# Optimization experiments

Measured on AMD Instinct MI355X. Metric: run time of the kernel, lower is better.

## Reference

```python
import jax, jax.numpy as jnp
import numpy as np
from jax.ops import segment_sum

N = 50000        # nodes
E = 800000       # edges (avg degree 16)
H = 128          # hidden_dim
N_ITER = 2       # BCRefinement n_iterations
TIE_P = 0.05     # fraction of tie (boundary) edges


def setup_inputs() -> dict:
    key = jax.random.key(0)
    ks = jax.random.split(key, 24)
    s = 0.02
    inp = {
        'h': jax.random.normal(ks[0], (N, H), jnp.float32),
        'e': jax.random.normal(ks[1], (E, H), jnp.float32),
        'edge_attr_raw': jax.random.normal(ks[2], (E, 10), jnp.float32),
        # edge_refine: Linear(3H,2H) -> ReLU -> Linear(2H,H)
        'W_er1': s * jax.random.normal(ks[3], (3 * H, 2 * H), jnp.float32),
        'b_er1': jnp.zeros((2 * H,), jnp.float32),
        'W_er2': s * jax.random.normal(ks[4], (2 * H, H), jnp.float32),
        'b_er2': jnp.zeros((H,), jnp.float32),
        # GRUCell(H,H) torch layout: [3H, H] chunks (r, z, n)
        'W_ih': s * jax.random.normal(ks[5], (3 * H, H), jnp.float32),
        'W_hh': s * jax.random.normal(ks[6], (3 * H, H), jnp.float32),
        'b_ih': jnp.zeros((3 * H,), jnp.float32),
        'b_hh': jnp.zeros((3 * H,), jnp.float32),
        # node_neigh_fc: Linear(H,H)
        'W_nn': s * jax.random.normal(ks[7], (H, H), jnp.float32),
        'b_nn': jnp.zeros((H,), jnp.float32),
        # gate_mlp: Linear(3H,H) -> ReLU -> Linear(H,1), last bias init -2.0
        'W_g1': s * jax.random.normal(ks[8], (3 * H, H), jnp.float32),
        'b_g1': jnp.zeros((H,), jnp.float32),
        'W_g2': s * jax.random.normal(ks[9], (H, 1), jnp.float32),
        'b_g2': jnp.full((1,), -2.0, jnp.float32),
        'edge_index': jax.random.randint(ks[10], (2, E), 0, N, jnp.int32),
        'is_tie': jax.random.uniform(ks[11], (E,)) < TIE_P,
    }
    return inp


def reference(h, e, edge_attr_raw,
              W_er1, b_er1, W_er2, b_er2,
              W_ih, W_hh, b_ih, b_hh,
              W_nn, b_nn,
              W_g1, b_g1, W_g2, b_g2,
              edge_index, is_tie):
    row = edge_index[0]
    col = edge_index[1]
    tie_f = is_tie.astype(h.dtype)                        # [E]
    internal = ~is_tie

    # coupling buses: endpoints of any tie edge (tie-incidence count > 0)
    cpl_cnt = segment_sum(tie_f, row, num_segments=N) + \
              segment_sum(tie_f, col, num_segments=N)     # [N]
    is_cpl = cpl_cnt > 0

    # internal edges pointing into coupling buses; b_smooth weights w = 1/sqrt(X^2+eps)
    to_cpl = internal & is_cpl[col]
    X = jnp.abs(edge_attr_raw[:, 1])
    w = jnp.where(to_cpl, 1.0 / jnp.sqrt(X * X + 1e-6), 0.0)
    w_den = segment_sum(w, col, num_segments=N)           # [N]
    w_norm = w / (w_den[col] + 1e-6)                      # [E], zero off-mask

    deg = jnp.maximum(cpl_cnt, 1.0)                       # clamp_min(1.0)

    h_work, e_work = h, e
    for _ in range(N_ITER):
        # --- tie-edge refinement (applied only on tie edges) ---
        edge_in = jnp.concatenate([e_work, h_work[row], h_work[col]], axis=-1)  # [E,3H]
        e_ref = jax.nn.relu(edge_in @ W_er1 + b_er1) @ W_er2 + b_er2            # [E,H]
        e_work = e_work + tie_f[:, None] * e_ref

        # --- node messages from internal neighbors into coupling buses ---
        m_node_msg = h_work[row] @ W_nn + b_nn                                   # [E,H]
        m_node_all = segment_sum(m_node_msg * w_norm[:, None], col,
                                 num_segments=N)                                 # [N,H]

        # --- mean of incident tie-edge features at each node ---
        tie_e = tie_f[:, None] * e_work                                          # [E,H]
        m_edge_all = (segment_sum(tie_e, row, num_segments=N) +
                      segment_sum(tie_e, col, num_segments=N)) / deg[:, None]    # [N,H]

        # --- gating + GRU update on coupling buses ---
        gate_in = jnp.concatenate([m_edge_all, m_node_all, h_work], axis=-1)     # [N,3H]
        gate = jax.nn.sigmoid(jax.nn.relu(gate_in @ W_g1 + b_g1) @ W_g2 + b_g2)  # [N,1]
        m = m_edge_all + gate * m_node_all                                       # [N,H]

        gi = m @ W_ih.T + b_ih                                                   # [N,3H]
        gh = h_work @ W_hh.T + b_hh
        r = jax.nn.sigmoid(gi[:, :H] + gh[:, :H])
        z = jax.nn.sigmoid(gi[:, H:2 * H] + gh[:, H:2 * H])
        n = jnp.tanh(gi[:, 2 * H:] + r * gh[:, 2 * H:])
        h_new = (1.0 - z) * n + z * h_work

        h_work = jnp.where(is_cpl[:, None], h_new, h_work)
    return h_work, e_work
```

## Files before the change

kernel.cpp:

```cpp
#include <hip/hip_runtime.h>
#include <cstdint>

#define N_NODES 50000
#define N_EDGES 800000
#define HDIM    128
#define TIE_CAP 44000
#define NITER   2
#define SCAN_B  256

typedef __attribute__((ext_vector_type(8))) short bf16x8;
typedef __attribute__((ext_vector_type(4))) float f32x4;

__device__ __forceinline__ uint32_t f2bf(float f) {
    uint32_t u = __builtin_bit_cast(uint32_t, f);
    return (u + 0x7fffu + ((u >> 16) & 1u)) >> 16;
}
__device__ __forceinline__ float bf2f(uint32_t b) {
    return __builtin_bit_cast(float, b << 16);
}
__device__ __forceinline__ uint32_t comb2(uint32_t me, uint32_t mn, float g) {
    float a0 = bf2f(me & 0xffffu) + g * bf2f(mn & 0xffffu);
    float a1 = bf2f(me >> 16)     + g * bf2f(mn >> 16);
    return f2bf(a0) | (f2bf(a1) << 16);
}


__device__ __forceinline__ void stage_a128(const float* __restrict__ base,
                                           const int* __restrict__ gidx,
                                           int m0, int Mlim, char* tile, int tid)
{
    const int c = tid & 15;
    #pragma unroll
    for (int p = 0; p < 4; ++p) {
        int row = p * 32 + (tid >> 4);
        int ar = m0 + row; if (ar >= Mlim) ar = Mlim - 1;
        long g = gidx ? gidx[ar] : ar;
        const float* s = base + g * HDIM + c * 4;
        float4 v0 = *(const float4*)s;
        float4 v1 = *(const float4*)(s + 64);
        uint2 w0 = make_uint2(f2bf(v0.x) | (f2bf(v0.y) << 16),
                              f2bf(v0.z) | (f2bf(v0.w) << 16));
        uint2 w1 = make_uint2(f2bf(v1.x) | (f2bf(v1.y) << 16),
                              f2bf(v1.z) | (f2bf(v1.w) << 16));
        int sw = (row & 7) << 4;
        *(uint2*)(tile + row * 256 + ((c * 8) ^ sw)) = w0;
        *(uint2*)(tile + row * 256 + ((c * 8 + 128) ^ sw)) = w1;
    }
}

__device__ __forceinline__ void stage_b128(const short* __restrict__ BT, int ldk,
                                           int n0, int k0, char* tile, int tid)
{
    const int c = tid & 15;
    #pragma unroll
    for (int p = 0; p < 4; ++p) {
        int n = p * 32 + (tid >> 4);
        uint4 v = *(const uint4*)&BT[(size_t)(n0 + n) * ldk + k0 + c * 8];
        *(uint4*)(tile + n * 256 + ((c * 16) ^ ((n & 7) << 4))) = v;
    }
}

__device__ __forceinline__ void mfma128(const char* At, const char* Bt,
                                        int wr, int wc, int lane, f32x4 acc[4][2])
{
    #pragma unroll
    for (int ks = 0; ks < 4; ++ks) {
        int kb = ks * 64 + (lane >> 4) * 16;
        bf16x8 aF[4], bF[2];
        #pragma unroll
        for (int mi = 0; mi < 4; ++mi) {
            int row = wr * 64 + mi * 16 + (lane & 15);
            aF[mi] = *(const bf16x8*)(At + row * 256 + (kb ^ ((row & 7) << 4)));
        }
        #pragma unroll
        for (int ni = 0; ni < 2; ++ni) {
            int n = wc * 32 + ni * 16 + (lane & 15);
            bF[ni] = *(const bf16x8*)(Bt + n * 256 + (kb ^ ((n & 7) << 4)));
        }
        #pragma unroll
        for (int mi = 0; mi < 4; ++mi)
            #pragma unroll
            for (int ni = 0; ni < 2; ++ni)
                acc[mi][ni] = __builtin_amdgcn_mfma_f32_16x16x32_bf16(
                    aF[mi], bF[ni], acc[mi][ni], 0, 0, 0);
    }
}

__global__ __launch_bounds__(512)
void k_tie_fused(float* __restrict__ out_e, const float* __restrict__ h,
                 const int* __restrict__ tie_cnt_p,
                 const int* __restrict__ tie_list, const int* __restrict__ tie_row,
                 const int* __restrict__ tie_col,
                 const short* __restrict__ BTer1, const short* __restrict__ BTer2,
                 const float* __restrict__ b_er1, const float* __restrict__ b_er2,
                 const float* __restrict__ deg_inv, float* __restrict__ m_edge)
{
    int cnt = *tie_cnt_p; if (cnt > TIE_CAP) cnt = TIE_CAP;
    const int m0 = blockIdx.x * 128;
    if (m0 >= cnt) return;

    __shared__ __align__(16) char At[32 * 1024];
    __shared__ __align__(16) char B0[32 * 1024];
    __shared__ __align__(16) char B1[32 * 1024];

    const int tid = threadIdx.x, lane = tid & 63;
    const int wid = tid >> 6, wr = wid >> 2, wc = wid & 3;

    f32x4 acc0[4][2] = {}, acc1[4][2] = {};
    #pragma unroll 1
    for (int c = 0; c < 3; ++c) {
        const float* base = (c == 0) ? out_e : h;
        const int* gi = (c == 0) ? tie_list : (c == 1) ? tie_row : tie_col;
        stage_a128(base, gi, m0, cnt, At, tid);
        stage_b128(BTer1, 384, 0,   c * 128, B0, tid);
        stage_b128(BTer1, 384, 128, c * 128, B1, tid);
        __syncthreads();
        mfma128(At, B0, wr, wc, lane, acc0);
        mfma128(At, B1, wr, wc, lane, acc1);
        __syncthreads();
    }

    #pragma unroll
    for (int half = 0; half < 2; ++half) {
        char* Ct = half ? B0 : At;
        #pragma unroll
        for (int ni = 0; ni < 2; ++ni) {
            int col = wc * 32 + ni * 16 + (lane & 15);
            float bv = b_er1[half * 128 + col];
            #pragma unroll
            for (int mi = 0; mi < 4; ++mi)
                #pragma unroll
                for (int j = 0; j < 4; ++j) {
                    int rl = wr * 64 + mi * 16 + ((lane >> 4) << 2) + j;
                    float v = fmaxf((half ? acc1 : acc0)[mi][ni][j] + bv, 0.f);
                    *(uint16_t*)(Ct + rl * 256 + ((col * 2) ^ ((rl & 7) << 4))) =
                        (uint16_t)f2bf(v);
                }
        }
    }
    stage_b128(BTer2, 256, 0, 0, B1, tid);
    __syncthreads();
    f32x4 acc2[4][2] = {};
    mfma128(At, B1, wr, wc, lane, acc2);
    __syncthreads();
    stage_b128(BTer2, 256, 0, 128, B1, tid);
    __syncthreads();
    mfma128(B0, B1, wr, wc, lane, acc2);

    int col0 = wc * 32 + (lane & 15);
    float bv0 = b_er2[col0], bv1 = b_er2[col0 + 16];
    #pragma unroll
    for (int mi = 0; mi < 4; ++mi) {
        #pragma unroll
        for (int j = 0; j < 4; ++j) {
            int i = m0 + wr * 64 + mi * 16 + ((lane >> 4) << 2) + j;
            if (i < cnt) {
                int e = tie_list[i], r = tie_row[i], cc = tie_col[i];
                float dr = deg_inv[r], dc = deg_inv[cc];
                #pragma unroll
                for (int ni = 0; ni < 2; ++ni) {
                    int col = col0 + ni * 16;
                    float er = acc2[mi][ni][j] + (ni ? bv1 : bv0);
                    size_t eb = (size_t)e * HDIM + col;
                    float v = out_e[eb] + er;
                    out_e[eb] = v;
                    atomicAdd(&m_edge[(size_t)r * HDIM + col], v * dr);
                    atomicAdd(&m_edge[(size_t)cc * HDIM + col], v * dc);
                }
            }
        }
    }
}

__global__ __launch_bounds__(512)
void k_hw(const float* __restrict__ h, const short* __restrict__ BTnn,
          const float* __restrict__ b_nn, float* __restrict__ HW)
{
    const int m0 = blockIdx.x * 128;
    __shared__ __align__(16) char At[32 * 1024];
    __shared__ __align__(16) char Bt[32 * 1024];
    const int tid = threadIdx.x, lane = tid & 63;
    const int wid = tid >> 6, wr = wid >> 2, wc = wid & 3;

    stage_a128(h, nullptr, m0, N_NODES, At, tid);
    stage_b128(BTnn, 128, 0, 0, Bt, tid);
    __syncthreads();
    f32x4 acc[4][2] = {};
    mfma128(At, Bt, wr, wc, lane, acc);

    #pragma unroll
    for (int ni = 0; ni < 2; ++ni) {
        int col = wc * 32 + ni * 16 + (lane & 15);
        float bv = b_nn[col];
        #pragma unroll
        for (int mi = 0; mi < 4; ++mi)
            #pragma unroll
            for (int j = 0; j < 4; ++j) {
                int row = m0 + wr * 64 + mi * 16 + ((lane >> 4) << 2) + j;
                if (row < N_NODES)
                    HW[(size_t)row * HDIM + col] = acc[mi][ni][j] + bv;
            }
    }
}

__global__ __launch_bounds__(512)
void k_node_mega(const float* __restrict__ m_edge, const float* __restrict__ m_node,
                 float* __restrict__ out_h, const float* __restrict__ cpl_cnt,
                 const short* __restrict__ BTg1, const float* __restrict__ b_g1,
                 const float* __restrict__ Wg2, const float* __restrict__ b_g2,
                 const short* __restrict__ BTcomb,
                 const short* __restrict__ BTihn, const short* __restrict__ BThhn,
                 const float* __restrict__ b_ih, const float* __restrict__ b_hh)
{
    const int m0 = blockIdx.x * 128;
    __shared__ __align__(16) char Tme[32 * 1024];
    __shared__ __align__(16) char Tmn[32 * 1024];
    __shared__ __align__(16) char Th [32 * 1024];
    __shared__ __align__(16) char Bt [32 * 1024];
    __shared__ float g_red[4][128];
    __shared__ float g_fin[128];

    const int tid = threadIdx.x, lane = tid & 63;
    const int wid = tid >> 6, wr = wid >> 2, wc = wid & 3;

    stage_a128(m_edge, nullptr, m0, N_NODES, Tme, tid);
    stage_a128(m_node, nullptr, m0, N_NODES, Tmn, tid);
    stage_a128(out_h,  nullptr, m0, N_NODES, Th,  tid);

    f32x4 accG[4][2] = {};
    #pragma unroll 1
    for (int c = 0; c < 3; ++c) {
        const char* Ac = (c == 0) ? Tme : (c == 1) ? Tmn : Th;
        stage_b128(BTg1, 384, 0, c * 128, Bt, tid);
        __syncthreads();
        mfma128(Ac, Bt, wr, wc, lane, accG);
        __syncthreads();
    }
    {
        float bg[2], wg[2];
        #pragma unroll
        for (int ni = 0; ni < 2; ++ni) {
            int col = wc * 32 + ni * 16 + (lane & 15);
            bg[ni] = b_g1[col]; wg[ni] = Wg2[col];
        }
        #pragma unroll
        for (int mi = 0; mi < 4; ++mi)
            #pragma unroll
            for (int j = 0; j < 4; ++j) {
                float p = fmaxf(accG[mi][0][j] + bg[0], 0.f) * wg[0]
                        + fmaxf(accG[mi][1][j] + bg[1], 0.f) * wg[1];
                #pragma unroll
                for (int o = 8; o; o >>= 1) p += __shfl_xor(p, o);
                if ((lane & 15) == 0)
                    g_red[wc][wr * 64 + mi * 16 + ((lane >> 4) << 2) + j] = p;
            }
    }
    __syncthreads();
    if (tid < 128) {
        float t = g_red[0][tid] + g_red[1][tid] + g_red[2][tid] + g_red[3][tid]
                + b_g2[0];
        g_fin[tid] = 1.f / (1.f + __expf(-t));
    }
    __syncthreads();

    {
        const int c = tid & 15;
        #pragma unroll
        for (int p = 0; p < 4; ++p) {
            int row = p * 32 + (tid >> 4);
            float g = g_fin[row];
            int sw = (row & 7) << 4;
            #pragma unroll
            for (int hh = 0; hh < 2; ++hh) {
                int off = (c * 8 + hh * 128) ^ sw;
                uint2 me2 = *(uint2*)(Tme + row * 256 + off);
                uint2 mn2 = *(uint2*)(Tmn + row * 256 + off);
                uint2 o2 = make_uint2(comb2(me2.x, mn2.x, g), comb2(me2.y, mn2.y, g));
                *(uint2*)(Tmn + row * 256 + off) = o2;
            }
        }
    }
    __syncthreads();

    f32x4 aR[4][2] = {}, aZ[4][2] = {}, aGI[4][2] = {}, aGH[4][2] = {};
    stage_b128(BTcomb, 256, 0, 0, Bt, tid);   __syncthreads();
    mfma128(Tmn, Bt, wr, wc, lane, aR);       __syncthreads();
    stage_b128(BTcomb, 256, 0, 128, Bt, tid); __syncthreads();
    mfma128(Th, Bt, wr, wc, lane, aR);        __syncthreads();
    stage_b128(BTcomb, 256, 128, 0, Bt, tid); __syncthreads();
    mfma128(Tmn, Bt, wr, wc, lane, aZ);       __syncthreads();
    stage_b128(BTcomb, 256, 128, 128, Bt, tid); __syncthreads();
    mfma128(Th, Bt, wr, wc, lane, aZ);        __syncthreads();
    stage_b128(BTihn, 128, 0, 0, Bt, tid);    __syncthreads();
    mfma128(Tmn, Bt, wr, wc, lane, aGI);      __syncthreads();
    stage_b128(BThhn, 128, 0, 0, Bt, tid);    __syncthreads();
    mfma128(Th, Bt, wr, wc, lane, aGH);

    #pragma unroll
    for (int ni = 0; ni < 2; ++ni) {
        int col = wc * 32 + ni * 16 + (lane & 15);
        float br  = b_ih[col] + b_hh[col];
        float bz  = b_ih[128 + col] + b_hh[128 + col];
        float bin = b_ih[256 + col], bhn = b_hh[256 + col];
        #pragma unroll
        for (int mi = 0; mi < 4; ++mi)
            #pragma unroll
            for (int j = 0; j < 4; ++j) {
                int node = m0 + wr * 64 + mi * 16 + ((lane >> 4) << 2) + j;
                if (node < N_NODES && cpl_cnt[node] > 0.f) {
                    float r = 1.f / (1.f + __expf(-(aR[mi][ni][j] + br)));
                    float z = 1.f / (1.f + __expf(-(aZ[mi][ni][j] + bz)));
                    float nn = tanhf(aGI[mi][ni][j] + bin + r * (aGH[mi][ni][j] + bhn));
                    size_t hb = (size_t)node * HDIM + col;
                    float hv = out_h[hb];
                    out_h[hb] = (1.f - z) * nn + z * hv;
                }
            }
    }
}

__global__ __launch_bounds__(256)
void k_prepw(const float* __restrict__ W, short* __restrict__ BT,
             int Kd, int Nd, int trans, int total)
{
    int i = blockIdx.x * 256 + threadIdx.x;
    if (i >= total) return;
    int n = i / Kd, k = i % Kd;
    float v = trans ? W[(size_t)k * Nd + n] : W[i];
    BT[i] = (short)f2bf(v);
}

__global__ __launch_bounds__(256)
void k_prepcomb(const float* __restrict__ W_ih, const float* __restrict__ W_hh,
                short* __restrict__ BTcomb)
{
    int i = blockIdx.x * 256 + threadIdx.x;
    if (i >= 256 * 256) return;
    int n = i >> 8, k = i & 255;
    float v = (k < 128) ? W_ih[n * 128 + k] : W_hh[n * 128 + (k - 128)];
    BTcomb[i] = (short)f2bf(v);
}

__global__ void k_detect(const uint8_t* __restrict__ tie_raw, int* __restrict__ fmt)
{
    __shared__ int cnt;
    if (threadIdx.x == 0) cnt = 0;
    __syncthreads();
    int c = 0;
    for (int i = threadIdx.x; i < 4096; i += 256)
        if ((i & 3) != 0 && tie_raw[i]) c++;
    if (c) atomicAdd(&cnt, c);
    __syncthreads();
    if (threadIdx.x == 0) *fmt = (cnt > 0) ? 1 : 0;
}

__device__ __forceinline__ bool is_tie_e(const void* raw, int fmt, int e)
{
    return fmt ? (((const uint8_t*)raw)[e] != 0) : (((const int*)raw)[e] != 0);
}

__global__ __launch_bounds__(256)
void k_tie(const void* __restrict__ tie_raw, const int* __restrict__ fmt_p,
           const int* __restrict__ ei, float* __restrict__ cpl_cnt,
           int* __restrict__ tie_cnt, int* __restrict__ tie_list,
           int* __restrict__ tie_row, int* __restrict__ tie_col)
{
    int e = blockIdx.x * 256 + threadIdx.x;
    if (e >= N_EDGES) return;
    if (!is_tie_e(tie_raw, *fmt_p, e)) return;
    int r = ei[e], c = ei[N_EDGES + e];
    atomicAdd(&cpl_cnt[r], 1.f);
    atomicAdd(&cpl_cnt[c], 1.f);
    int idx = atomicAdd(tie_cnt, 1);
    if (idx < TIE_CAP) { tie_list[idx] = e; tie_row[idx] = r; tie_col[idx] = c; }
}

__global__ __launch_bounds__(256)
void k_w(const void* __restrict__ tie_raw, const int* __restrict__ fmt_p,
         const int* __restrict__ ei, const float* __restrict__ attr,
         const float* __restrict__ cpl_cnt, float* __restrict__ w_den,
         float* __restrict__ w_arr, int* __restrict__ hist)
{
    int e = blockIdx.x * 256 + threadIdx.x;
    if (e >= N_EDGES) return;
    float w = 0.f;
    if (!is_tie_e(tie_raw, *fmt_p, e)) {
        int c = ei[N_EDGES + e];
        if (cpl_cnt[c] > 0.f) {
            float X = fabsf(attr[(size_t)e * 10 + 1]);
            w = 1.f / sqrtf(X * X + 1e-6f);
            atomicAdd(&w_den[c], w);
            atomicAdd(&hist[c], 1);
        }
    }
    w_arr[e] = w;
}

__global__ __launch_bounds__(256)
void k_wnorm(const int* __restrict__ ei, const float* __restrict__ w_den,
             float* __restrict__ w_arr)
{
    int e = blockIdx.x * 256 + threadIdx.x;
    if (e >= N_EDGES) return;
    float w = w_arr[e];
    if (w != 0.f) {
        int c = ei[N_EDGES + e];
        w_arr[e] = w / (w_den[c] + 1e-6f);
    }
}

__global__ __launch_bounds__(256)
void k_deg(const float* __restrict__ cpl_cnt, float* __restrict__ deg_inv)
{
    int n = blockIdx.x * 256 + threadIdx.x;
    if (n >= N_NODES) return;
    deg_inv[n] = 1.f / fmaxf(cpl_cnt[n], 1.f);
}

__global__ __launch_bounds__(SCAN_B)
void k_scan1(const int* __restrict__ cnt, int* __restrict__ excl,
             int* __restrict__ bsum, int n)
{
    __shared__ int s[SCAN_B];
    int t = threadIdx.x;
    int i = blockIdx.x * SCAN_B + t;
    int v = (i < n) ? cnt[i] : 0;
    s[t] = v;
    __syncthreads();
    for (int o = 1; o < SCAN_B; o <<= 1) {
        int u = (t >= o) ? s[t - o] : 0;
        __syncthreads();
        s[t] += u;
        __syncthreads();
    }
    if (i < n) excl[i] = s[t] - v;
    if (t == SCAN_B - 1) bsum[blockIdx.x] = s[t];
}

__global__ void k_scan2(int* __restrict__ bsum, int nb, int* __restrict__ total)
{
    if (threadIdx.x == 0) {
        int run = 0;
        for (int b = 0; b < nb; ++b) { int x = bsum[b]; bsum[b] = run; run += x; }
        *total = run;
    }
}

__global__ __launch_bounds__(256)
void k_scan3(const int* __restrict__ excl, const int* __restrict__ bsum,
             int* __restrict__ row_ptr, int* __restrict__ cursor,
             const int* __restrict__ total, int n)
{
    int i = blockIdx.x * 256 + threadIdx.x;
    if (i < n) {
        int v = excl[i] + bsum[i >> 8];
        row_ptr[i] = v;
        cursor[i] = v;
    }
    if (i == n) row_ptr[n] = *total;
}

__global__ __launch_bounds__(256)
void k_fill(const int* __restrict__ ei, const float* __restrict__ w_arr,
            int* __restrict__ cursor, int* __restrict__ csr_row,
            float* __restrict__ csr_w)
{
    int e = blockIdx.x * 256 + threadIdx.x;
    if (e >= N_EDGES) return;
    float w = w_arr[e];
    if (w == 0.f) return;
    int c = ei[N_EDGES + e];
    int pos = atomicAdd(&cursor[c], 1);
    csr_row[pos] = ei[e];
    csr_w[pos] = w;
}

__global__ __launch_bounds__(256)
void k_mnode_csr(const int* __restrict__ row_ptr, const int* __restrict__ csr_row,
                 const float* __restrict__ csr_w, const float* __restrict__ hW,
                 float* __restrict__ m_node)
{
    int n = blockIdx.x * 4 + (threadIdx.x >> 6);
    if (n >= N_NODES) return;
    int lane = threadIdx.x & 63;
    int s = row_ptr[n], t = row_ptr[n + 1];
    float a0 = 0.f, a1 = 0.f;
    for (int j = s; j < t; ++j) {
        int r = csr_row[j];
        float w = csr_w[j];
        a0 += w * hW[(size_t)r * HDIM + lane];
        a1 += w * hW[(size_t)r * HDIM + 64 + lane];
    }
    m_node[(size_t)n * HDIM + lane] = a0;
    m_node[(size_t)n * HDIM + 64 + lane] = a1;
}

extern "C" void kernel_launch(void* const* d_in, const int* in_sizes, int n_in,
                              void* d_out, int out_size, void* d_ws, size_t ws_size,
                              hipStream_t stream)
{
    const float* h     = (const float*)d_in[0];
    const float* e     = (const float*)d_in[1];
    const float* attr  = (const float*)d_in[2];
    const float* W_er1 = (const float*)d_in[3];
    const float* b_er1 = (const float*)d_in[4];
    const float* W_er2 = (const float*)d_in[5];
    const float* b_er2 = (const float*)d_in[6];
    const float* W_ih  = (const float*)d_in[7];
    const float* W_hh  = (const float*)d_in[8];
    const float* b_ih  = (const float*)d_in[9];
    const float* b_hh  = (const float*)d_in[10];
    const float* W_nn  = (const float*)d_in[11];
    const float* b_nn  = (const float*)d_in[12];
    const float* W_g1  = (const float*)d_in[13];
    const float* b_g1  = (const float*)d_in[14];
    const float* W_g2  = (const float*)d_in[15];
    const float* b_g2  = (const float*)d_in[16];
    const int*   ei    = (const int*)d_in[17];
    const void*  tie_raw = d_in[18];

    float* out_h = (float*)d_out;
    float* out_e = out_h + (size_t)N_NODES * HDIM;

    char* ws = (char*)d_ws;
    size_t off = 0;
    auto alloc = [&](size_t bytes) -> void* {
        void* p = ws + off;
        off = (off + bytes + 255) & ~(size_t)255;
        return p;
    };
    float* cpl_cnt = (float*)alloc((size_t)N_NODES * 4);
    float* w_den   = (float*)alloc((size_t)N_NODES * 4);
    int*   hist    = (int*)  alloc((size_t)N_NODES * 4);
    int*   counters= (int*)  alloc(256);
    size_t zero_bytes = off;
    float* deg_inv = (float*)alloc((size_t)N_NODES * 4);
    float* w_arr   = (float*)alloc((size_t)N_EDGES * 4);
    int* tie_list  = (int*)alloc((size_t)TIE_CAP * 4);
    int* tie_row   = (int*)alloc((size_t)TIE_CAP * 4);
    int* tie_col   = (int*)alloc((size_t)TIE_CAP * 4);
    short* BTer1   = (short*)alloc((size_t)256 * 384 * 2);
    short* BTer2   = (short*)alloc((size_t)128 * 256 * 2);
    short* BTnn    = (short*)alloc((size_t)128 * 128 * 2);
    short* BTg1    = (short*)alloc((size_t)128 * 384 * 2);
    short* BTcomb  = (short*)alloc((size_t)256 * 256 * 2);
    short* BTihn   = (short*)alloc((size_t)128 * 128 * 2);
    short* BThhn   = (short*)alloc((size_t)128 * 128 * 2);
    float* HW      = (float*)alloc((size_t)N_NODES * HDIM * 4);
    float* m_edge  = (float*)alloc((size_t)N_NODES * HDIM * 4);
    float* m_node  = (float*)alloc((size_t)N_NODES * HDIM * 4);
    int* excl      = (int*)alloc((size_t)N_NODES * 4);
    int* bsum      = (int*)alloc(256 * 4);
    int* row_ptr   = (int*)alloc((size_t)(N_NODES + 1) * 4);
    int* cursor    = (int*)alloc((size_t)N_NODES * 4);
    int* csr_row   = (int*)alloc((size_t)N_EDGES * 4);
    float* csr_w   = (float*)alloc((size_t)N_EDGES * 4);
    if (off > ws_size) return;

    int* fmt_p     = counters;
    int* tie_cnt   = counters + 1;
    int* csr_total = counters + 2;

    const int EB   = N_EDGES / 256;
    const int GM_T = (TIE_CAP + 127) / 128;
    const int GM_N = (N_NODES + 127) / 128;
    const int NB   = (N_NODES + SCAN_B - 1) / SCAN_B;

    hipMemsetAsync(d_ws, 0, zero_bytes, stream);
    k_detect<<<1, 256, 0, stream>>>((const uint8_t*)tie_raw, fmt_p);
    hipMemcpyAsync(out_h, h, (size_t)N_NODES * HDIM * 4, hipMemcpyDeviceToDevice, stream);
    hipMemcpyAsync(out_e, e, (size_t)N_EDGES * HDIM * 4, hipMemcpyDeviceToDevice, stream);

    k_prepw<<<(384*256+255)/256, 256, 0, stream>>>(W_er1, BTer1, 384, 256, 1, 384*256);
    k_prepw<<<(256*128+255)/256, 256, 0, stream>>>(W_er2, BTer2, 256, 128, 1, 256*128);
    k_prepw<<<(128*128+255)/256, 256, 0, stream>>>(W_nn,  BTnn,  128, 128, 1, 128*128);
    k_prepw<<<(384*128+255)/256, 256, 0, stream>>>(W_g1,  BTg1,  384, 128, 1, 384*128);
    k_prepcomb<<<(256*256+255)/256, 256, 0, stream>>>(W_ih, W_hh, BTcomb);
    k_prepw<<<(128*128+255)/256, 256, 0, stream>>>(W_ih + 256*128, BTihn, 128, 128, 0, 128*128);
    k_prepw<<<(128*128+255)/256, 256, 0, stream>>>(W_hh + 256*128, BThhn, 128, 128, 0, 128*128);

    k_tie<<<EB, 256, 0, stream>>>(tie_raw, fmt_p, ei, cpl_cnt, tie_cnt, tie_list, tie_row, tie_col);
    k_w<<<EB, 256, 0, stream>>>(tie_raw, fmt_p, ei, attr, cpl_cnt, w_den, w_arr, hist);
    k_wnorm<<<EB, 256, 0, stream>>>(ei, w_den, w_arr);
    k_deg<<<(N_NODES + 255) / 256, 256, 0, stream>>>(cpl_cnt, deg_inv);

    k_scan1<<<NB, SCAN_B, 0, stream>>>(hist, excl, bsum, N_NODES);
    k_scan2<<<1, 64, 0, stream>>>(bsum, NB, csr_total);
    k_scan3<<<(N_NODES + 256) / 256, 256, 0, stream>>>(excl, bsum, row_ptr, cursor, csr_total, N_NODES);
    k_fill<<<EB, 256, 0, stream>>>(ei, w_arr, cursor, csr_row, csr_w);

    for (int it = 0; it < NITER; ++it) {
        hipMemsetAsync(m_edge, 0, (size_t)N_NODES * HDIM * 4, stream);
        k_tie_fused<<<GM_T, 512, 0, stream>>>(
            out_e, out_h, tie_cnt, tie_list, tie_row, tie_col,
            BTer1, BTer2, b_er1, b_er2, deg_inv, m_edge);
        k_hw<<<GM_N, 512, 0, stream>>>(out_h, BTnn, b_nn, HW);
        k_mnode_csr<<<(N_NODES + 3) / 4, 256, 0, stream>>>(row_ptr, csr_row, csr_w, HW, m_node);
        k_node_mega<<<GM_N, 512, 0, stream>>>(
            m_edge, m_node, out_h, cpl_cnt,
            BTg1, b_g1, W_g2, b_g2, BTcomb, BTihn, BThhn, b_ih, b_hh);
    }
}
```

Before: 962.4 us.

## Aggregate raw bf16 node states before linear layer and fuse W_nn into node kernel

Reorders the neighbor message computation from aggregate(h W_nn + b) to (aggregate h) W_nn + sumw*b. This removes the separate k_hw GEMM and its fp32 HW write and read. The W_nn matmul now runs inside k_node_mega on the aggregated tile, and a bf16 copy of h is kept up to date so the gather and tie kernels read half the bytes. The cost is extra bf16 rounding of h and of the aggregate, plus one more GEMM stage and extra syncs in the node kernel.

```diff
diff --git a/kernel.cpp b/kernel.cpp
--- a/kernel.cpp
+++ b/kernel.cpp
@@ -48,6 +48,21 @@
     }
 }
 
+__device__ __forceinline__ void stage_bf128(const uint16_t* __restrict__ base,
+                                            const int* __restrict__ gidx,
+                                            int m0, int Mlim, char* tile, int tid)
+{
+    const int c = tid & 15;
+    #pragma unroll
+    for (int p = 0; p < 4; ++p) {
+        int row = p * 32 + (tid >> 4);
+        int ar = m0 + row; if (ar >= Mlim) ar = Mlim - 1;
+        long g = gidx ? gidx[ar] : ar;
+        uint4 v = *(const uint4*)(base + g * HDIM + c * 8);
+        *(uint4*)(tile + row * 256 + ((c * 16) ^ ((row & 7) << 4))) = v;
+    }
+}
+
 __device__ __forceinline__ void stage_b128(const short* __restrict__ BT, int ldk,
                                            int n0, int k0, char* tile, int tid)
 {
@@ -87,7 +102,7 @@
 }
 
 __global__ __launch_bounds__(512)
-void k_tie_fused(float* __restrict__ out_e, const float* __restrict__ h,
+void k_tie_fused(float* __restrict__ out_e, const uint16_t* __restrict__ h_bf,
                  const int* __restrict__ tie_cnt_p,
                  const int* __restrict__ tie_list, const int* __restrict__ tie_row,
                  const int* __restrict__ tie_col,
@@ -109,9 +124,8 @@
     f32x4 acc0[4][2] = {}, acc1[4][2] = {};
     #pragma unroll 1
     for (int c = 0; c < 3; ++c) {
-        const float* base = (c == 0) ? out_e : h;
-        const int* gi = (c == 0) ? tie_list : (c == 1) ? tie_row : tie_col;
-        stage_a128(base, gi, m0, cnt, At, tid);
+        if (c == 0) stage_a128(out_e, tie_list, m0, cnt, At, tid);
+        else        stage_bf128(h_bf, (c == 1) ? tie_row : tie_col, m0, cnt, At, tid);
         stage_b128(BTer1, 384, 0,   c * 128, B0, tid);
         stage_b128(BTer1, 384, 128, c * 128, B1, tid);
         __syncthreads();
@@ -173,39 +187,10 @@
 }
 
 __global__ __launch_bounds__(512)
-void k_hw(const float* __restrict__ h, const short* __restrict__ BTnn,
-          const float* __restrict__ b_nn, float* __restrict__ HW)
-{
-    const int m0 = blockIdx.x * 128;
-    __shared__ __align__(16) char At[32 * 1024];
-    __shared__ __align__(16) char Bt[32 * 1024];
-    const int tid = threadIdx.x, lane = tid & 63;
-    const int wid = tid >> 6, wr = wid >> 2, wc = wid & 3;
-
-    stage_a128(h, nullptr, m0, N_NODES, At, tid);
-    stage_b128(BTnn, 128, 0, 0, Bt, tid);
-    __syncthreads();
-    f32x4 acc[4][2] = {};
-    mfma128(At, Bt, wr, wc, lane, acc);
-
-    #pragma unroll
-    for (int ni = 0; ni < 2; ++ni) {
-        int col = wc * 32 + ni * 16 + (lane & 15);
-        float bv = b_nn[col];
-        #pragma unroll
-        for (int mi = 0; mi < 4; ++mi)
-            #pragma unroll
-            for (int j = 0; j < 4; ++j) {
-                int row = m0 + wr * 64 + mi * 16 + ((lane >> 4) << 2) + j;
-                if (row < N_NODES)
-                    HW[(size_t)row * HDIM + col] = acc[mi][ni][j] + bv;
-            }
-    }
-}
-
-__global__ __launch_bounds__(512)
-void k_node_mega(const float* __restrict__ m_edge, const float* __restrict__ m_node,
-                 float* __restrict__ out_h, const float* __restrict__ cpl_cnt,
+void k_node_mega(const float* __restrict__ m_edge, const uint16_t* __restrict__ agg,
+                 float* __restrict__ out_h, uint16_t* __restrict__ h_bf,
+                 const float* __restrict__ cpl_cnt, const float* __restrict__ sumw,
+                 const short* __restrict__ BTnn, const float* __restrict__ b_nn,
                  const short* __restrict__ BTg1, const float* __restrict__ b_g1,
                  const float* __restrict__ Wg2, const float* __restrict__ b_g2,
                  const short* __restrict__ BTcomb,
@@ -219,13 +204,41 @@
     __shared__ __align__(16) char Bt [32 * 1024];
     __shared__ float g_red[4][128];
     __shared__ float g_fin[128];
+    __shared__ float sw_s[128];
 
     const int tid = threadIdx.x, lane = tid & 63;
     const int wid = tid >> 6, wr = wid >> 2, wc = wid & 3;
 
     stage_a128(m_edge, nullptr, m0, N_NODES, Tme, tid);
-    stage_a128(m_node, nullptr, m0, N_NODES, Tmn, tid);
-    stage_a128(out_h,  nullptr, m0, N_NODES, Th,  tid);
+    stage_bf128(agg,   nullptr, m0, N_NODES, Tmn, tid);
+    stage_bf128(h_bf,  nullptr, m0, N_NODES, Th,  tid);
+    stage_b128(BTnn, 128, 0, 0, Bt, tid);
+    if (tid < 128) {
+        int n = m0 + tid; if (n >= N_NODES) n = N_NODES - 1;
+        sw_s[tid] = sumw[n];
+    }
+    __syncthreads();
+
+    {
+        f32x4 accM[4][2] = {};
+        mfma128(Tmn, Bt, wr, wc, lane, accM);
+        __syncthreads();
+        #pragma unroll
+        for (int ni = 0; ni < 2; ++ni) {
+            int col = wc * 32 + ni * 16 + (lane & 15);
+            float bv = b_nn[col];
+            #pragma unroll
+            for (int mi = 0; mi < 4; ++mi)
+                #pragma unroll
+                for (int j = 0; j < 4; ++j) {
+                    int rl = wr * 64 + mi * 16 + ((lane >> 4) << 2) + j;
+                    float v = accM[mi][ni][j] + sw_s[rl] * bv;
+                    *(uint16_t*)(Tmn + rl * 256 + ((col * 2) ^ ((rl & 7) << 4))) =
+                        (uint16_t)f2bf(v);
+                }
+        }
+        __syncthreads();
+    }
 
     f32x4 accG[4][2] = {};
     #pragma unroll 1
@@ -313,10 +326,32 @@
                     float nn = tanhf(aGI[mi][ni][j] + bin + r * (aGH[mi][ni][j] + bhn));
                     size_t hb = (size_t)node * HDIM + col;
                     float hv = out_h[hb];
-                    out_h[hb] = (1.f - z) * nn + z * hv;
+                    float hn = (1.f - z) * nn + z * hv;
+                    out_h[hb] = hn;
+                    h_bf[hb] = (uint16_t)f2bf(hn);
                 }
             }
     }
+}
+
+__global__ __launch_bounds__(256)
+void k_mnode_gather(const int* __restrict__ row_ptr, const int* __restrict__ csr_row,
+                    const float* __restrict__ csr_w, const uint16_t* __restrict__ h_bf,
+                    uint16_t* __restrict__ agg)
+{
+    int n = blockIdx.x * 4 + (threadIdx.x >> 6);
+    if (n >= N_NODES) return;
+    int lane = threadIdx.x & 63;
+    int s = row_ptr[n], t = row_ptr[n + 1];
+    float a0 = 0.f, a1 = 0.f;
+    for (int j = s; j < t; ++j) {
+        int r = csr_row[j];
+        float w = csr_w[j];
+        uint32_t v = *(const uint32_t*)(h_bf + (size_t)r * HDIM + lane * 2);
+        a0 += w * bf2f(v & 0xffffu);
+        a1 += w * bf2f(v >> 16);
+    }
+    *(uint32_t*)(agg + (size_t)n * HDIM + lane * 2) = f2bf(a0) | (f2bf(a1) << 16);
 }
 
 __global__ __launch_bounds__(256)
@@ -339,6 +374,15 @@
     int n = i >> 8, k = i & 255;
     float v = (k < 128) ? W_ih[n * 128 + k] : W_hh[n * 128 + (k - 128)];
     BTcomb[i] = (short)f2bf(v);
+}
+
+__global__ __launch_bounds__(256)
+void k_h2bf(const float* __restrict__ h, uint16_t* __restrict__ h_bf)
+{
+    int i = blockIdx.x * 256 + threadIdx.x;
+    if (i >= N_NODES * HDIM / 2) return;
+    float2 v = *(const float2*)(h + (size_t)i * 2);
+    *(uint32_t*)(h_bf + (size_t)i * 2) = f2bf(v.x) | (f2bf(v.y) << 16);
 }
 
 __global__ void k_detect(const uint8_t* __restrict__ tie_raw, int* __restrict__ fmt)
@@ -410,11 +454,14 @@
 }
 
 __global__ __launch_bounds__(256)
-void k_deg(const float* __restrict__ cpl_cnt, float* __restrict__ deg_inv)
+void k_deg(const float* __restrict__ cpl_cnt, const float* __restrict__ w_den,
+           float* __restrict__ deg_inv, float* __restrict__ sumw)
 {
     int n = blockIdx.x * 256 + threadIdx.x;
     if (n >= N_NODES) return;
     deg_inv[n] = 1.f / fmaxf(cpl_cnt[n], 1.f);
+    float wd = w_den[n];
+    sumw[n] = wd / (wd + 1e-6f);
 }
 
 __global__ __launch_bounds__(SCAN_B)
@@ -473,26 +520,6 @@
     int pos = atomicAdd(&cursor[c], 1);
     csr_row[pos] = ei[e];
     csr_w[pos] = w;
-}
-
-__global__ __launch_bounds__(256)
-void k_mnode_csr(const int* __restrict__ row_ptr, const int* __restrict__ csr_row,
-                 const float* __restrict__ csr_w, const float* __restrict__ hW,
-                 float* __restrict__ m_node)
-{
-    int n = blockIdx.x * 4 + (threadIdx.x >> 6);
-    if (n >= N_NODES) return;
-    int lane = threadIdx.x & 63;
-    int s = row_ptr[n], t = row_ptr[n + 1];
-    float a0 = 0.f, a1 = 0.f;
-    for (int j = s; j < t; ++j) {
-        int r = csr_row[j];
-        float w = csr_w[j];
-        a0 += w * hW[(size_t)r * HDIM + lane];
-        a1 += w * hW[(size_t)r * HDIM + 64 + lane];
-    }
-    m_node[(size_t)n * HDIM + lane] = a0;
-    m_node[(size_t)n * HDIM + 64 + lane] = a1;
 }
 
 extern "C" void kernel_launch(void* const* d_in, const int* in_sizes, int n_in,
@@ -535,6 +562,7 @@
     int*   counters= (int*)  alloc(256);
     size_t zero_bytes = off;
     float* deg_inv = (float*)alloc((size_t)N_NODES * 4);
+    float* sumw    = (float*)alloc((size_t)N_NODES * 4);
     float* w_arr   = (float*)alloc((size_t)N_EDGES * 4);
     int* tie_list  = (int*)alloc((size_t)TIE_CAP * 4);
     int* tie_row   = (int*)alloc((size_t)TIE_CAP * 4);
@@ -546,9 +574,9 @@
     short* BTcomb  = (short*)alloc((size_t)256 * 256 * 2);
     short* BTihn   = (short*)alloc((size_t)128 * 128 * 2);
     short* BThhn   = (short*)alloc((size_t)128 * 128 * 2);
-    float* HW      = (float*)alloc((size_t)N_NODES * HDIM * 4);
+    uint16_t* h_bf = (uint16_t*)alloc((size_t)N_NODES * HDIM * 2);
+    uint16_t* agg  = (uint16_t*)alloc((size_t)N_NODES * HDIM * 2);
     float* m_edge  = (float*)alloc((size_t)N_NODES * HDIM * 4);
-    float* m_node  = (float*)alloc((size_t)N_NODES * HDIM * 4);
     int* excl      = (int*)alloc((size_t)N_NODES * 4);
     int* bsum      = (int*)alloc(256 * 4);
     int* row_ptr   = (int*)alloc((size_t)(N_NODES + 1) * 4);
@@ -570,6 +598,7 @@
     k_detect<<<1, 256, 0, stream>>>((const uint8_t*)tie_raw, fmt_p);
     hipMemcpyAsync(out_h, h, (size_t)N_NODES * HDIM * 4, hipMemcpyDeviceToDevice, stream);
     hipMemcpyAsync(out_e, e, (size_t)N_EDGES * HDIM * 4, hipMemcpyDeviceToDevice, stream);
+    k_h2bf<<<(N_NODES * HDIM / 2 + 255) / 256, 256, 0, stream>>>(h, h_bf);
 
     k_prepw<<<(384*256+255)/256, 256, 0, stream>>>(W_er1, BTer1, 384, 256, 1, 384*256);
     k_prepw<<<(256*128+255)/256, 256, 0, stream>>>(W_er2, BTer2, 256, 128, 1, 256*128);
@@ -582,7 +611,7 @@
     k_tie<<<EB, 256, 0, stream>>>(tie_raw, fmt_p, ei, cpl_cnt, tie_cnt, tie_list, tie_row, tie_col);
     k_w<<<EB, 256, 0, stream>>>(tie_raw, fmt_p, ei, attr, cpl_cnt, w_den, w_arr, hist);
     k_wnorm<<<EB, 256, 0, stream>>>(ei, w_den, w_arr);
-    k_deg<<<(N_NODES + 255) / 256, 256, 0, stream>>>(cpl_cnt, deg_inv);
+    k_deg<<<(N_NODES + 255) / 256, 256, 0, stream>>>(cpl_cnt, w_den, deg_inv, sumw);
 
     k_scan1<<<NB, SCAN_B, 0, stream>>>(hist, excl, bsum, N_NODES);
     k_scan2<<<1, 64, 0, stream>>>(bsum, NB, csr_total);
@@ -592,12 +621,12 @@
     for (int it = 0; it < NITER; ++it) {
         hipMemsetAsync(m_edge, 0, (size_t)N_NODES * HDIM * 4, stream);
         k_tie_fused<<<GM_T, 512, 0, stream>>>(
-            out_e, out_h, tie_cnt, tie_list, tie_row, tie_col,
+            out_e, h_bf, tie_cnt, tie_list, tie_row, tie_col,
             BTer1, BTer2, b_er1, b_er2, deg_inv, m_edge);
-        k_hw<<<GM_N, 512, 0, stream>>>(out_h, BTnn, b_nn, HW);
-        k_mnode_csr<<<(N_NODES + 3) / 4, 256, 0, stream>>>(row_ptr, csr_row, csr_w, HW, m_node);
+        k_mnode_gather<<<(N_NODES + 3) / 4, 256, 0, stream>>>(row_ptr, csr_row, csr_w, h_bf, agg);
         k_node_mega<<<GM_N, 512, 0, stream>>>(
-            m_edge, m_node, out_h, cpl_cnt,
-            BTg1, b_g1, W_g2, b_g2, BTcomb, BTihn, BThhn, b_ih, b_hh);
-    }
-}
+            m_edge, agg, out_h, h_bf, cpl_cnt, sumw,
+            BTnn, b_nn, BTg1, b_g1, W_g2, b_g2,
+            BTcomb, BTihn, BThhn, b_ih, b_hh);
+    }
+}
```

New measurement: 949.4 us. About the same (-1.3%).
